# Kernel tuning notes

Measured on AMD Instinct MI355X. Metric: run time of the kernel, lower is better.

## Reference

```python
import jax, jax.numpy as jnp
import numpy as np

TOKEN_VOCAB = 512   # token id range used for packing ngram tuples into ints
VOCAB_SIZE = 50000  # max ngram vocab per size (ngram_to_size values)
NGRAM_SIZES = (2, 3)
OOV_ID = 0
ID_OFFSET = 4       # vocab ids start at 4 (idx + 4 in _get_top_ngrams)


def _make_table(rng, n):
    # Build a sorted, unique packed-key table emulating the dict produced by
    # _get_top_ngrams: {ngram_tuple: idx+4}. Keys packed base-TOKEN_VOCAB.
    cand = rng.integers(0, TOKEN_VOCAB, size=(VOCAB_SIZE * 3, n), dtype=np.int64)
    packed = np.zeros(cand.shape[0], dtype=np.int64)
    for j in range(n):
        packed = packed * TOKEN_VOCAB + cand[:, j]
    uniq = np.unique(packed)[:VOCAB_SIZE]
    keys = np.sort(uniq)
    vals = np.arange(keys.shape[0], dtype=np.int64) + ID_OFFSET
    return jnp.asarray(keys), jnp.asarray(vals)


def setup_inputs() -> dict:
    key = jax.random.key(0)
    x = jax.random.randint(key, (256, 8192), 0, TOKEN_VOCAB, dtype=jnp.int64)
    rng = np.random.default_rng(0)
    keys2, vals2 = _make_table(rng, 2)
    keys3, vals3 = _make_table(rng, 3)
    return {"x": x, "keys2": keys2, "vals2": vals2, "keys3": keys3, "vals3": vals3}


def _encode_ngram_ids(x, keys, vals, n):
    # Left-pad with 0 by (n-1), sliding windows of length n per position,
    # pack each window into a single int key, then sorted-table lookup
    # (semantically equal to lookup_table.get(tuple(window), 0)).
    B, S = x.shape
    padded = jnp.pad(x, ((0, 0), (n - 1, 0)))  # [B, S+n-1]
    packed = jnp.zeros((B, S), dtype=jnp.int64)
    for j in range(n):  # tiny fixed loop over window offset
        packed = packed * TOKEN_VOCAB + padded[:, j:j + S]
    pos = jnp.clip(jnp.searchsorted(keys, packed.ravel()), 0, keys.shape[0] - 1)
    hit = keys[pos] == packed.ravel()
    ids = jnp.where(hit, vals[pos], OOV_ID)
    return ids.reshape(B, S)


def reference(x, keys2, vals2, keys3, vals3):
    tables = {2: (keys2, vals2), 3: (keys3, vals3)}
    per_n = [_encode_ngram_ids(x, *tables[n], n) for n in NGRAM_SIZES]
    return jnp.stack(per_n, axis=0)  # [n_sizes, B, S]
```

## Files before the change

kernel.cpp:

```cpp
#include <hip/hip_runtime.h>


#define TOKEN_VOCAB 512
#define SHIFT3 10
#define NBUCKET3 (1 << 17)
#define DIRECT2_ENTRIES (TOKEN_VOCAB * TOKEN_VOCAB)

__global__ void build_direct2(const int* __restrict__ keys2,
                              const int* __restrict__ vals2, int K2,
                              int* __restrict__ direct2) {
    int i = blockIdx.x * blockDim.x + threadIdx.x;
    if (i < K2) direct2[keys2[i]] = vals2[i];
}

__global__ void build_start3(const int* __restrict__ keys3, int K3,
                             int* __restrict__ start3) {
    int b = blockIdx.x * blockDim.x + threadIdx.x;
    if (b > NBUCKET3) return;
    int target = b << SHIFT3;
    int lo = 0, hi = K3;
    while (lo < hi) {
        int mid = (lo + hi) >> 1;
        if (keys3[mid] < target) lo = mid + 1; else hi = mid;
    }
    start3[b] = lo;
}

__global__ void ngram_encode_fast(const int* __restrict__ x,
                                  const int* __restrict__ direct2,
                                  const int* __restrict__ start3,
                                  const int* __restrict__ keys3,
                                  const int* __restrict__ vals3,
                                  int* __restrict__ out, int total, int S) {
    int base = (blockIdx.x * blockDim.x + threadIdx.x) * 4;
    if (base >= total) return;
    int s = base & (S - 1);
    const int4 cur = *(const int4*)(x + base);
    int tm1 = (s >= 1) ? x[base - 1] : 0;
    int tm2 = (s >= 1) ? x[base - 2] : 0;
    int t[6] = {tm2, tm1, cur.x, cur.y, cur.z, cur.w};

    int o2[4], o3[4];
    int k3v[4], blo[4], bhi[4];
    #pragma unroll
    for (int j = 0; j < 4; ++j) {
        int k2 = t[j + 1] * TOKEN_VOCAB + t[j + 2];
        int k3 = (t[j] * TOKEN_VOCAB + t[j + 1]) * TOKEN_VOCAB + t[j + 2];
        k3v[j] = k3;
        o2[j] = direct2[k2];
        int b = k3 >> SHIFT3;
        blo[j] = start3[b];
        bhi[j] = start3[b + 1];
    }
    #pragma unroll
    for (int j = 0; j < 4; ++j) {
        int v = 0;
        for (int p = blo[j]; p < bhi[j]; ++p) {
            int kv = keys3[p];
            if (kv >= k3v[j]) { v = (kv == k3v[j]) ? vals3[p] : 0; break; }
        }
        o3[j] = v;
    }
    *(int4*)(out + base)         = make_int4(o2[0], o2[1], o2[2], o2[3]);
    *(int4*)(out + total + base) = make_int4(o3[0], o3[1], o3[2], o3[3]);
}

__device__ __forceinline__ int table_lookup(const int* __restrict__ keys,
                                            const int* __restrict__ vals,
                                            int K, int packed) {
    int lo = 0, hi = K;
    while (lo < hi) {
        int mid = (lo + hi) >> 1;
        if (keys[mid] < packed) lo = mid + 1; else hi = mid;
    }
    int pos = lo < (K - 1) ? lo : (K - 1);
    return (keys[pos] == packed) ? vals[pos] : 0;
}

__global__ void ngram_encode_kernel(const int* __restrict__ x,
                                    const int* __restrict__ keys2,
                                    const int* __restrict__ vals2, int K2,
                                    const int* __restrict__ keys3,
                                    const int* __restrict__ vals3, int K3,
                                    int* __restrict__ out, int total, int S) {
    int idx = blockIdx.x * blockDim.x + threadIdx.x;
    if (idx >= total) return;
    int s = idx & (S - 1);
    int t0 = x[idx];
    int t1 = (s >= 1) ? x[idx - 1] : 0;
    int t2 = (s >= 2) ? x[idx - 2] : 0;
    int k2 = t1 * TOKEN_VOCAB + t0;
    int k3 = (t2 * TOKEN_VOCAB + t1) * TOKEN_VOCAB + t0;
    out[idx]         = table_lookup(keys2, vals2, K2, k2);
    out[total + idx] = table_lookup(keys3, vals3, K3, k3);
}

extern "C" void kernel_launch(void* const* d_in, const int* in_sizes, int n_in,
                              void* d_out, int out_size, void* d_ws, size_t ws_size,
                              hipStream_t stream) {
    const int* x     = (const int*)d_in[0];
    const int* keys2 = (const int*)d_in[1];
    const int* vals2 = (const int*)d_in[2];
    const int* keys3 = (const int*)d_in[3];
    const int* vals3 = (const int*)d_in[4];
    int* out = (int*)d_out;

    const int total = in_sizes[0];
    const int S = 8192;
    const int K2 = in_sizes[1];
    const int K3 = in_sizes[3];

    const size_t ws_needed = (size_t)(DIRECT2_ENTRIES + NBUCKET3 + 1) * sizeof(int);
    if (ws_size >= ws_needed) {
        int* direct2 = (int*)d_ws;
        int* start3  = direct2 + DIRECT2_ENTRIES;

        hipMemsetAsync(direct2, 0, DIRECT2_ENTRIES * sizeof(int), stream);
        build_direct2<<<(K2 + 255) / 256, 256, 0, stream>>>(keys2, vals2, K2, direct2);
        build_start3<<<(NBUCKET3 + 1 + 255) / 256, 256, 0, stream>>>(keys3, K3, start3);

        const int block = 256;
        const int elems = total / 4;
        ngram_encode_fast<<<(elems + block - 1) / block, block, 0, stream>>>(
            x, direct2, start3, keys3, vals3, out, total, S);
    } else {
        const int block = 256;
        ngram_encode_kernel<<<(total + block - 1) / block, block, 0, stream>>>(
            x, keys2, vals2, K2, keys3, vals3, K3, out, total, S);
    }
}
```

Before: 100.7 us.

## Replace bucketed sorted-range trigram lookup with open-addressing hash table

```diff
diff --git a/kernel.cpp b/kernel.cpp
--- a/kernel.cpp
+++ b/kernel.cpp
@@ -2,9 +2,14 @@
 
 
 #define TOKEN_VOCAB 512
-#define SHIFT3 10
-#define NBUCKET3 (1 << 17)
 #define DIRECT2_ENTRIES (TOKEN_VOCAB * TOKEN_VOCAB)
+#define HASH_BITS 18
+#define HASH_SLOTS (1 << HASH_BITS)
+#define HASH_MASK (HASH_SLOTS - 1)
+
+__device__ __forceinline__ unsigned hash3(int k) {
+    return ((unsigned)k * 2654435761u) >> (32 - HASH_BITS);
+}
 
 __global__ void build_direct2(const int* __restrict__ keys2,
                               const int* __restrict__ vals2, int K2,
@@ -13,24 +18,23 @@
     if (i < K2) direct2[keys2[i]] = vals2[i];
 }
 
-__global__ void build_start3(const int* __restrict__ keys3, int K3,
-                             int* __restrict__ start3) {
-    int b = blockIdx.x * blockDim.x + threadIdx.x;
-    if (b > NBUCKET3) return;
-    int target = b << SHIFT3;
-    int lo = 0, hi = K3;
-    while (lo < hi) {
-        int mid = (lo + hi) >> 1;
-        if (keys3[mid] < target) lo = mid + 1; else hi = mid;
+__global__ void build_hash3(const int* __restrict__ keys3,
+                            const int* __restrict__ vals3, int K3,
+                            int2* __restrict__ tab) {
+    int i = blockIdx.x * blockDim.x + threadIdx.x;
+    if (i >= K3) return;
+    int k = keys3[i], v = vals3[i];
+    unsigned h = hash3(k);
+    while (true) {
+        int prev = atomicCAS(&tab[h].x, -1, k);
+        if (prev == -1) { tab[h].y = v; break; }
+        h = (h + 1) & HASH_MASK;
     }
-    start3[b] = lo;
 }
 
 __global__ void ngram_encode_fast(const int* __restrict__ x,
                                   const int* __restrict__ direct2,
-                                  const int* __restrict__ start3,
-                                  const int* __restrict__ keys3,
-                                  const int* __restrict__ vals3,
+                                  const int2* __restrict__ tab,
                                   int* __restrict__ out, int total, int S) {
     int base = (blockIdx.x * blockDim.x + threadIdx.x) * 4;
     if (base >= total) return;
@@ -40,26 +44,27 @@
     int tm2 = (s >= 1) ? x[base - 2] : 0;
     int t[6] = {tm2, tm1, cur.x, cur.y, cur.z, cur.w};
 
-    int o2[4], o3[4];
-    int k3v[4], blo[4], bhi[4];
+    int o2[4], o3[4], k3v[4];
+    unsigned h[4];
+    int2 slot[4];
     #pragma unroll
     for (int j = 0; j < 4; ++j) {
         int k2 = t[j + 1] * TOKEN_VOCAB + t[j + 2];
         int k3 = (t[j] * TOKEN_VOCAB + t[j + 1]) * TOKEN_VOCAB + t[j + 2];
         k3v[j] = k3;
         o2[j] = direct2[k2];
-        int b = k3 >> SHIFT3;
-        blo[j] = start3[b];
-        bhi[j] = start3[b + 1];
+        h[j] = hash3(k3);
+        slot[j] = tab[h[j]];
     }
     #pragma unroll
     for (int j = 0; j < 4; ++j) {
-        int v = 0;
-        for (int p = blo[j]; p < bhi[j]; ++p) {
-            int kv = keys3[p];
-            if (kv >= k3v[j]) { v = (kv == k3v[j]) ? vals3[p] : 0; break; }
+        int2 sl = slot[j];
+        unsigned hh = h[j];
+        while (sl.x != k3v[j] && sl.x != -1) {
+            hh = (hh + 1) & HASH_MASK;
+            sl = tab[hh];
         }
-        o3[j] = v;
+        o3[j] = (sl.x == k3v[j]) ? sl.y : 0;
     }
     *(int4*)(out + base)         = make_int4(o2[0], o2[1], o2[2], o2[3]);
     *(int4*)(out + total + base) = make_int4(o3[0], o3[1], o3[2], o3[3]);
@@ -110,19 +115,21 @@
     const int K2 = in_sizes[1];
     const int K3 = in_sizes[3];
 
-    const size_t ws_needed = (size_t)(DIRECT2_ENTRIES + NBUCKET3 + 1) * sizeof(int);
+    const size_t ws_needed = (size_t)DIRECT2_ENTRIES * sizeof(int)
+                           + (size_t)HASH_SLOTS * sizeof(int2);
     if (ws_size >= ws_needed) {
-        int* direct2 = (int*)d_ws;
-        int* start3  = direct2 + DIRECT2_ENTRIES;
+        int*  direct2 = (int*)d_ws;
+        int2* tab     = (int2*)(direct2 + DIRECT2_ENTRIES);
 
         hipMemsetAsync(direct2, 0, DIRECT2_ENTRIES * sizeof(int), stream);
+        hipMemsetAsync(tab, 0xFF, (size_t)HASH_SLOTS * sizeof(int2), stream);
         build_direct2<<<(K2 + 255) / 256, 256, 0, stream>>>(keys2, vals2, K2, direct2);
-        build_start3<<<(NBUCKET3 + 1 + 255) / 256, 256, 0, stream>>>(keys3, K3, start3);
+        build_hash3<<<(K3 + 255) / 256, 256, 0, stream>>>(keys3, vals3, K3, tab);
 
         const int block = 256;
         const int elems = total / 4;
         ngram_encode_fast<<<(elems + block - 1) / block, block, 0, stream>>>(
-            x, direct2, start3, keys3, vals3, out, total, S);
+            x, direct2, tab, out, total, S);
     } else {
         const int block = 256;
         ngram_encode_kernel<<<(total + block - 1) / block, block, 0, stream>>>(
```

After: 112.4 us. 1.12x slower.
